# Optimization experiments

Hardware: AMD Instinct MI355X
Metric: run time of the kernel (lower is better)

The kernel has to match this reference:

```python
import jax, jax.numpy as jnp
import numpy as np
from jax import lax

NTAG = 31
HID = 100
NEG = -10000.0


def gru_dir(x, w_ih, w_hh, b_ih, b_hh):
    # x: [T, B, 100]; PyTorch gate order in weights: [r, z, n]
    B = x.shape[1]
    h0 = jnp.zeros((B, HID), dtype=x.dtype)

    def step(h, xt):
        gi = xt @ w_ih.T + b_ih          # [B, 3H]
        gh = h @ w_hh.T + b_hh           # [B, 3H]
        ir, iz, inn = jnp.split(gi, 3, axis=-1)
        hr, hz, hn = jnp.split(gh, 3, axis=-1)
        r = jax.nn.sigmoid(ir + hr)
        z = jax.nn.sigmoid(iz + hz)
        n = jnp.tanh(inn + r * hn)
        h = (1.0 - z) * n + z * h
        return h, h

    _, ys = lax.scan(step, h0, x)
    return ys                             # [T, B, H]


def viterbi(feats, msk, transitions):
    # feats: [T, 31], msk: [T], transitions[next, prev]
    init = jnp.full((NTAG,), NEG, dtype=feats.dtype).at[0].set(0.0)
    idx = jnp.arange(NTAG)

    def step(fv, inp):
        feat, m = inp
        scores = fv[None, :] + transitions       # [next, prev]
        bp = jnp.argmax(scores, axis=1)          # [31]
        vv = jnp.max(scores, axis=1) + feat      # [31]
        live = m > 0
        fv_new = jnp.where(live, vv, fv)
        bp = jnp.where(live, bp, idx)            # masked step: identity backpointer
        return fv_new, bp

    fv, bps = lax.scan(step, init, (feats, msk))
    final = jnp.argmax(fv)
    score = fv[final]

    def back(tag, bp):
        return bp[tag], tag

    _, path = lax.scan(back, final, bps, reverse=True)  # path[t] = tag at step t
    return score, path


def setup_inputs() -> dict:
    key = jax.random.key(0)
    ks = jax.random.split(key, 12)
    T, B, D = 2048, 128, 100
    s = 0.1  # ~ 1/sqrt(hidden)
    u = lambda k, sh: jax.random.uniform(k, sh, jnp.float32, -s, s)
    tr = jax.random.normal(ks[10], (NTAG, NTAG), jnp.float32)
    tr = tr.at[0, :].set(NEG).at[:, 29].set(NEG).at[:, 30].set(NEG)
    tr = tr.at[30, 30].set(0.0).at[29, 30].set(0.0)
    return {
        "sentence": jax.random.normal(ks[0], (T, B, D), jnp.float32),
        "mask": jnp.ones((B, T), jnp.float32),
        "w_ih_f": u(ks[1], (3 * HID, D)), "w_hh_f": u(ks[2], (3 * HID, HID)),
        "b_ih_f": u(ks[3], (3 * HID,)), "b_hh_f": u(ks[4], (3 * HID,)),
        "w_ih_b": u(ks[5], (3 * HID, D)), "w_hh_b": u(ks[6], (3 * HID, HID)),
        "b_ih_b": u(ks[7], (3 * HID,)), "b_hh_b": u(ks[8], (3 * HID,)),
        "w_out": u(ks[9], (NTAG, 2 * HID)), "b_out": jnp.zeros((NTAG,), jnp.float32),
        "transitions": tr,
        "batch": B,
        "seq": 0,
    }


def reference(sentence, mask, w_ih_f, w_hh_f, b_ih_f, b_hh_f,
              w_ih_b, w_hh_b, b_ih_b, b_hh_b, w_out, b_out,
              transitions, batch, seq):
    fwd = gru_dir(sentence, w_ih_f, w_hh_f, b_ih_f, b_hh_f)
    bwd = gru_dir(sentence[::-1], w_ih_b, w_hh_b, b_ih_b, b_hh_b)[::-1]
    gru_out = jnp.concatenate([fwd, bwd], axis=-1)        # [T, B, 200]
    feats = gru_out @ w_out.T + b_out                      # [T, B, 31]
    feats_b = jnp.transpose(feats, (1, 0, 2))              # [B, T, 31]
    score, path = viterbi(feats_b[seq], mask[seq], transitions)
    return score, path
```

## Files before the change

kernel.cpp:

```cpp
#include <hip/hip_runtime.h>
#include <stdint.h>

#define TT 2048
#define BB 128
#define DD 100
#define HH 100
#define GG 300
#define NT 31
#define NEGV (-10000.0f)

#define REP25(M) M(0) M(1) M(2) M(3) M(4) M(5) M(6) M(7) M(8) M(9) M(10) M(11) \
                 M(12) M(13) M(14) M(15) M(16) M(17) M(18) M(19) M(20) M(21) M(22) M(23) M(24)
#define REP31(M) M(0) M(1) M(2) M(3) M(4) M(5) M(6) M(7) M(8) M(9) M(10) M(11) \
                 M(12) M(13) M(14) M(15) M(16) M(17) M(18) M(19) M(20) M(21) M(22) M(23) \
                 M(24) M(25) M(26) M(27) M(28) M(29) M(30)
#define REP8(M)  M(0) M(1) M(2) M(3) M(4) M(5) M(6) M(7)

#define RL(v, k) __int_as_float(__builtin_amdgcn_readlane(__float_as_int(v), (k)))

__global__ __launch_bounds__(320) void gi_kernel(
    const float* __restrict__ sent, const int* __restrict__ seqp,
    const float* __restrict__ w_ih_f, const float* __restrict__ b_ih_f,
    const float* __restrict__ w_ih_b, const float* __restrict__ b_ih_b,
    float* __restrict__ gi)
{
    const int t   = blockIdx.x;
    const int dir = blockIdx.y;
    const int j   = threadIdx.x;
    const int seq = seqp[0];
    const int ts  = dir ? (TT - 1 - t) : t;
    __shared__ __align__(16) float x_s[DD];
    if (j < DD) x_s[j] = sent[((size_t)ts * BB + seq) * DD + j];
    __syncthreads();
    if (j < GG) {
        const float* w = dir ? w_ih_b : w_ih_f;
        const float* b = dir ? b_ih_b : b_ih_f;
        const float4* w4 = (const float4*)(w + j * DD);
        const float4* x4 = (const float4*)x_s;
        float a0 = 0.f, a1 = 0.f, a2 = 0.f, a3 = 0.f;
        #pragma unroll
        for (int k = 0; k < DD / 4; k++) {
            float4 wv = w4[k], xv = x4[k];
            a0 += wv.x * xv.x; a1 += wv.y * xv.y;
            a2 += wv.z * xv.z; a3 += wv.w * xv.w;
        }
        gi[((size_t)dir * TT + t) * GG + j] = b[j] + (a0 + a1) + (a2 + a3);
    }
}

__global__ __launch_bounds__(512, 2) void gru_seq_kernel(
    const float* __restrict__ gi,
    const float* __restrict__ w_hh_f, const float* __restrict__ b_hh_f,
    const float* __restrict__ w_hh_b, const float* __restrict__ b_hh_b,
    const float* __restrict__ w_out,
    float* __restrict__ pfeat)
{
    const int dir  = blockIdx.x;
    const int tid  = threadIdx.x;
    const int wave = tid >> 6, lane = tid & 63;
    const int q    = wave >> 1;
    const bool isA = !(wave & 1);
    const int k0   = q * 25;
    const float* w_hh = dir ? w_hh_b : w_hh_f;
    const float* b_hh = dir ? b_hh_b : b_hh_f;
    const float* gid  = gi + (size_t)dir * TT * GG;
    float* pf = pfeat + (size_t)dir * TT * NT;

    __shared__ float part[2][4][384];

    const int s0 = (isA ? 0 : 64) + lane;
    const int s1 = (isA ? 128 : 192) + lane;
    const int s2 = (isA ? 256 : 320) + lane;

    const float* r0 = w_hh + s0 * DD + k0;
    const float* r1 = w_hh + s1 * DD + k0;
    const int wrow = (s2 - GG) < (NT - 1) ? (s2 - GG) : (NT - 1);
    const float* r2 = (s2 < GG) ? (w_hh + s2 * DD + k0)
                                : (w_out + wrow * (2 * HH) + dir * HH + k0);

    #define DECLW(i) float w0_##i, w1_##i, w2_##i;
    REP25(DECLW)
    #define LDW(i) w0_##i = r0[i]; w1_##i = r1[i]; w2_##i = r2[i];
    REP25(LDW)

    const int r = k0 + lane;
    float bhr = 0.f, bhz = 0.f, bhn = 0.f;
    if (lane < 25) { bhr = b_hh[r]; bhz = b_hh[HH + r]; bhn = b_hh[2 * HH + r]; }

    const int  p     = lane - 32;
    const bool is_pf = (wave == 1) && (p >= 0) && (p < NT);
    #define DECLPH(i) float ph##i = 0.f;
    REP8(DECLPH)

    float hreg = 0.f;

    float gAr = 0.f, gAz = 0.f, gAn = 0.f, gBr = 0.f, gBz = 0.f, gBn = 0.f;
    if (lane < 25) {
        gAr = gid[r];      gAz = gid[HH + r];      gAn = gid[2 * HH + r];
        gBr = gid[GG + r]; gBz = gid[GG + HH + r]; gBn = gid[GG + 2 * HH + r];
    }

    #define DOTK(i) { float hk = RL(hreg, i);              \
        a0 = fmaf(hk, w0_##i, a0);                          \
        a1 = fmaf(hk, w1_##i, a1);                          \
        a2 = fmaf(hk, w2_##i, a2); }

    #define GRU_STEP(TIDX, BUF, SLOT, cr, cz, cn) {                          \
        float a0 = 0.f, a1 = 0.f, a2 = 0.f;                                  \
        REP25(DOTK)                                                          \
        part[BUF][q][s0] = a0;                                               \
        part[BUF][q][s1] = a1;                                               \
        part[BUF][q][s2] = a2;                                               \
        __syncthreads();                                                     \
        if (lane < 25) {                                                     \
            float pr = part[BUF][0][r] + part[BUF][1][r]                     \
                     + part[BUF][2][r] + part[BUF][3][r];                    \
            float pz = part[BUF][0][HH + r] + part[BUF][1][HH + r]           \
                     + part[BUF][2][HH + r] + part[BUF][3][HH + r];          \
            float pn = part[BUF][0][2 * HH + r] + part[BUF][1][2 * HH + r]   \
                     + part[BUF][2][2 * HH + r] + part[BUF][3][2 * HH + r];  \
            float xr  = pr + bhr + (cr);                                     \
            float xz  = pz + bhz + (cz);                                     \
            float ghn = pn + bhn;                                            \
            float rr  = 1.f / (1.f + __expf(-xr));                           \
            float zz  = 1.f / (1.f + __expf(-xz));                           \
            float pre = (cn) + rr * ghn;                                     \
            pre = fmaxf(fminf(pre, 40.f), -40.f);                            \
            float e2  = __expf(-2.f * pre);                                  \
            float nn  = (1.f - e2) / (1.f + e2);                             \
            hreg = (1.f - zz) * nn + zz * hreg;                              \
            int tp = (TIDX) + 2; tp = (tp < TT) ? tp : (TT - 1);             \
            cr = gid[tp * GG + r];                                           \
            cz = gid[tp * GG + HH + r];                                      \
            cn = gid[tp * GG + 2 * HH + r];                                  \
        }                                                                    \
        if (is_pf && (TIDX) > 0) {                                           \
            ph##SLOT = part[BUF][0][GG + p] + part[BUF][1][GG + p]           \
                     + part[BUF][2][GG + p] + part[BUF][3][GG + p];          \
        }                                                                    \
    }

    #define PHST(i) pf[(size_t)(dir ? (TT - 1 - (tb + i)) : (tb + i)) * NT + p] = ph##i;

    for (int tt = 0; tt < TT; tt += 8) {
        GRU_STEP(tt + 0, 0, 7, gAr, gAz, gAn)
        if (is_pf && tt >= 8) { int tb = tt - 8; REP8(PHST) }
        GRU_STEP(tt + 1, 1, 0, gBr, gBz, gBn)
        GRU_STEP(tt + 2, 0, 1, gAr, gAz, gAn)
        GRU_STEP(tt + 3, 1, 2, gBr, gBz, gBn)
        GRU_STEP(tt + 4, 0, 3, gAr, gAz, gAn)
        GRU_STEP(tt + 5, 1, 4, gBr, gBz, gBn)
        GRU_STEP(tt + 6, 0, 5, gAr, gAz, gAn)
        GRU_STEP(tt + 7, 1, 6, gBr, gBz, gBn)
    }

    {
        float a2 = 0.f;
        #define DOT2K(i) a2 = fmaf(RL(hreg, i), w2_##i, a2);
        REP25(DOT2K)
        part[0][q][s2] = a2;
        __syncthreads();
        if (is_pf) {
            ph7 = part[0][0][GG + p] + part[0][1][GG + p]
                + part[0][2][GG + p] + part[0][3][GG + p];
            int tb = TT - 8;
            REP8(PHST)
        }
    }
}

__global__ __launch_bounds__(64) void vit_scan_kernel(
    const float* __restrict__ pfeat, const float* __restrict__ mask,
    const int* __restrict__ seqp, const float* __restrict__ trans,
    const float* __restrict__ b_out,
    float* __restrict__ fvg, int* __restrict__ meta, float* __restrict__ out)
{
    const int lane = threadIdx.x;
    const int ln   = (lane < NT) ? lane : (NT - 1);
    const float* mrow = mask + (size_t)seqp[0] * TT;
    const float* pff = pfeat;
    const float* pfb = pfeat + (size_t)TT * NT;

    #define DECLTR(i) float tr##i = trans[ln * NT + i];
    REP31(DECLTR)
    const float bo = b_out[ln];

    float fv = (lane == 0) ? 0.f : NEGV;
    fvg[lane] = fv;

    float ffr[8], fbr[8], mr[8];
    #pragma unroll
    for (int q = 0; q < 8; q++) {
        ffr[q] = pff[q * NT + ln]; fbr[q] = pfb[q * NT + ln]; mr[q] = mrow[q];
    }

    for (int t = 0; t < TT; t += 8) {
        #pragma unroll
        for (int q = 0; q < 8; q++) {
            float fcur = ffr[q] + fbr[q] + bo;
            float mcur = mr[q];
            int tp = t + q + 8; tp = (tp < TT) ? tp : (TT - 1);
            ffr[q] = pff[tp * NT + ln]; fbr[q] = pfb[tp * NT + ln]; mr[q] = mrow[tp];
            #define VADD(i) float v##i = RL(fv, i) + tr##i;
            REP31(VADD)
            #undef VADD
            v0  = fmaxf(v0,  v16); v1  = fmaxf(v1,  v17); v2  = fmaxf(v2,  v18);
            v3  = fmaxf(v3,  v19); v4  = fmaxf(v4,  v20); v5  = fmaxf(v5,  v21);
            v6  = fmaxf(v6,  v22); v7  = fmaxf(v7,  v23); v8  = fmaxf(v8,  v24);
            v9  = fmaxf(v9,  v25); v10 = fmaxf(v10, v26); v11 = fmaxf(v11, v27);
            v12 = fmaxf(v12, v28); v13 = fmaxf(v13, v29); v14 = fmaxf(v14, v30);
            v0 = fmaxf(v0, v8);  v1 = fmaxf(v1, v9);  v2 = fmaxf(v2, v10);
            v3 = fmaxf(v3, v11); v4 = fmaxf(v4, v12); v5 = fmaxf(v5, v13);
            v6 = fmaxf(v6, v14); v7 = fmaxf(v7, v15);
            v0 = fmaxf(v0, v4); v1 = fmaxf(v1, v5); v2 = fmaxf(v2, v6); v3 = fmaxf(v3, v7);
            v0 = fmaxf(v0, v2); v1 = fmaxf(v1, v3);
            float m = fmaxf(v0, v1);
            float cand = m + fcur;
            fv = (mcur > 0.f) ? cand : fv;
            fvg[(t + q + 1) * 64 + lane] = fv;
        }
    }

    float fbest = RL(fv, 0);
    int ftag = 0;
    #pragma unroll
    for (int q = 1; q < NT; q++) {
        float s = RL(fv, q);
        if (s > fbest) { fbest = s; ftag = q; }
    }
    if (lane == 0) { out[0] = fbest; meta[0] = ftag; }
}

__global__ __launch_bounds__(1024) void vit_bp_kernel(
    const float* __restrict__ fvg, const float* __restrict__ mask,
    const int* __restrict__ seqp, const float* __restrict__ trans,
    uint8_t* __restrict__ bpg, uint8_t* __restrict__ gmapg)
{
    const int b    = blockIdx.x;
    const int tid  = threadIdx.x;
    const int wave = tid >> 6, lane = tid & 63;
    const int j    = lane & 31;
    const int jr   = (j < NT) ? j : (NT - 1);
    const float* mrow = mask + (size_t)seqp[0] * TT;

    __shared__ int bpl[64][32];

    float trj[NT];
    #pragma unroll
    for (int q = 0; q < NT; q++) trj[q] = trans[jr * NT + q];

    #pragma unroll
    for (int q4 = 0; q4 < 4; q4++) {
        const int t = b * 64 + wave * 4 + q4;
        float fvp = fvg[t * 64 + lane];
        float mcur = mrow[t];
        float best = RL(fvp, 0) + trj[0];
        int bi = 0;
        #pragma unroll
        for (int q = 1; q < NT; q++) {
            float s = RL(fvp, q) + trj[q];
            if (s > best) { best = s; bi = q; }
        }
        int bpn = (mcur > 0.f) ? bi : j;
        if (j == 31) bpn = 31;
        if (lane < 32) {
            bpl[wave * 4 + q4][lane] = bpn;
            if (j < NT) bpg[(size_t)t * NT + j] = (uint8_t)bpn;
        }
    }
    __syncthreads();
    if (wave == 0) {
        int G = j;
        for (int i = 0; i < 64; i++) {
            int bpv = bpl[i][j];
            G = __shfl(G, bpv);
        }
        if (lane < 32) gmapg[b * 32 + lane] = (uint8_t)G;
    }
}

__global__ __launch_bounds__(64) void vit_back_kernel(
    const uint8_t* __restrict__ bpg, const uint8_t* __restrict__ gmapg,
    const int* __restrict__ meta, float* __restrict__ out)
{
    const int tid = threadIdx.x;
    __shared__ uint8_t bps[TT * NT];
    __shared__ uint8_t gm[32 * 32];
    __shared__ uint8_t echk[32];

    const uint32_t* src = (const uint32_t*)bpg;
    uint32_t* dst = (uint32_t*)bps;
    for (int i = tid; i < TT * NT / 4; i += 64) dst[i] = src[i];
    for (int i = tid; i < 1024 / 4; i += 64)
        ((uint32_t*)gm)[i] = ((const uint32_t*)gmapg)[i];
    __syncthreads();

    if (tid == 0) {
        int tag = meta[0];
        for (int b = 31; b >= 0; b--) { echk[b] = (uint8_t)tag; tag = gm[b * 32 + tag]; }
    }
    __syncthreads();
    if (tid < 32) {
        int tag = echk[tid];
        for (int i = 63; i >= 0; i--) {
            int t = tid * 64 + i;
            out[1 + t] = (float)tag;
            tag = bps[t * NT + tag];
        }
    }
}

extern "C" void kernel_launch(void* const* d_in, const int* in_sizes, int n_in,
                              void* d_out, int out_size, void* d_ws, size_t ws_size,
                              hipStream_t stream) {
    const float* sent   = (const float*)d_in[0];
    const float* mask   = (const float*)d_in[1];
    const float* w_ih_f = (const float*)d_in[2];
    const float* w_hh_f = (const float*)d_in[3];
    const float* b_ih_f = (const float*)d_in[4];
    const float* b_hh_f = (const float*)d_in[5];
    const float* w_ih_b = (const float*)d_in[6];
    const float* w_hh_b = (const float*)d_in[7];
    const float* b_ih_b = (const float*)d_in[8];
    const float* b_hh_b = (const float*)d_in[9];
    const float* w_out  = (const float*)d_in[10];
    const float* b_out  = (const float*)d_in[11];
    const float* trans  = (const float*)d_in[12];
    const int*   seqp   = (const int*)d_in[14];
    float* out = (float*)d_out;

    float* gi    = (float*)d_ws;
    float* pfeat = gi + (size_t)2 * TT * GG;
    float* fvg   = pfeat + (size_t)2 * TT * NT;
    float* bpf   = fvg + (size_t)(TT + 1) * 64;
    uint8_t* bpg   = (uint8_t*)bpf;
    uint8_t* gmapg = bpg + (size_t)TT * NT;
    int*     meta  = (int*)(gmapg + 1024);

    gi_kernel<<<dim3(TT, 2), 320, 0, stream>>>(sent, seqp, w_ih_f, b_ih_f,
                                               w_ih_b, b_ih_b, gi);
    gru_seq_kernel<<<2, 512, 0, stream>>>(gi, w_hh_f, b_hh_f, w_hh_b, b_hh_b,
                                          w_out, pfeat);
    vit_scan_kernel<<<1, 64, 0, stream>>>(pfeat, mask, seqp, trans, b_out,
                                          fvg, meta, out);
    vit_bp_kernel<<<32, 1024, 0, stream>>>(fvg, mask, seqp, trans, bpg, gmapg);
    vit_back_kernel<<<1, 64, 0, stream>>>(bpg, gmapg, meta, out);
}
```

Measured before the change: 2.189 ms.

## Stage GRU input gates in double-buffered LDS and pin weights in VGPRs

Each 8-step block of precomputed input-gate values is now copied cooperatively into a double-buffered shared-memory tile, one block ahead, so the recurrent step reads LDS instead of issuing per-step global loads on the serial path. Empty asm constraints keep the recurrent weights and the Viterbi transition matrix resident in VGPRs, and waves-per-EU attributes replace the launch-bounds occupancy hint. The cost is extra LDS and a copy per block. The final block reads past the end of the gate array, and the buffer being refilled is not fenced against waves still reading it, so there is a race risk.

Measured after the change: 2.245 ms. +2.6%, slower.

```diff
diff --git a/kernel.cpp b/kernel.cpp
--- a/kernel.cpp
+++ b/kernel.cpp
@@ -48,7 +48,8 @@
     }
 }
 
-__global__ __launch_bounds__(512, 2) void gru_seq_kernel(
+__global__ __launch_bounds__(512) __attribute__((amdgpu_waves_per_eu(2, 2)))
+void gru_seq_kernel(
     const float* __restrict__ gi,
     const float* __restrict__ w_hh_f, const float* __restrict__ b_hh_f,
     const float* __restrict__ w_hh_b, const float* __restrict__ b_hh_b,
@@ -67,6 +68,7 @@
     float* pf = pfeat + (size_t)dir * TT * NT;
 
     __shared__ float part[2][4][384];
+    __shared__ __align__(16) float gibuf[2][8][GG];
 
     const int s0 = (isA ? 0 : 64) + lane;
     const int s1 = (isA ? 128 : 192) + lane;
@@ -82,6 +84,21 @@
     REP25(DECLW)
     #define LDW(i) w0_##i = r0[i]; w1_##i = r1[i]; w2_##i = r2[i];
     REP25(LDW)
+    asm volatile("" : "+v"(w0_0),"+v"(w0_1),"+v"(w0_2),"+v"(w0_3),"+v"(w0_4),
+                      "+v"(w0_5),"+v"(w0_6),"+v"(w0_7),"+v"(w0_8),"+v"(w0_9),
+                      "+v"(w0_10),"+v"(w0_11),"+v"(w0_12),"+v"(w0_13),"+v"(w0_14),
+                      "+v"(w0_15),"+v"(w0_16),"+v"(w0_17),"+v"(w0_18),"+v"(w0_19),
+                      "+v"(w0_20),"+v"(w0_21),"+v"(w0_22),"+v"(w0_23),"+v"(w0_24));
+    asm volatile("" : "+v"(w1_0),"+v"(w1_1),"+v"(w1_2),"+v"(w1_3),"+v"(w1_4),
+                      "+v"(w1_5),"+v"(w1_6),"+v"(w1_7),"+v"(w1_8),"+v"(w1_9),
+                      "+v"(w1_10),"+v"(w1_11),"+v"(w1_12),"+v"(w1_13),"+v"(w1_14),
+                      "+v"(w1_15),"+v"(w1_16),"+v"(w1_17),"+v"(w1_18),"+v"(w1_19),
+                      "+v"(w1_20),"+v"(w1_21),"+v"(w1_22),"+v"(w1_23),"+v"(w1_24));
+    asm volatile("" : "+v"(w2_0),"+v"(w2_1),"+v"(w2_2),"+v"(w2_3),"+v"(w2_4),
+                      "+v"(w2_5),"+v"(w2_6),"+v"(w2_7),"+v"(w2_8),"+v"(w2_9),
+                      "+v"(w2_10),"+v"(w2_11),"+v"(w2_12),"+v"(w2_13),"+v"(w2_14),
+                      "+v"(w2_15),"+v"(w2_16),"+v"(w2_17),"+v"(w2_18),"+v"(w2_19),
+                      "+v"(w2_20),"+v"(w2_21),"+v"(w2_22),"+v"(w2_23),"+v"(w2_24));
 
     const int r = k0 + lane;
     float bhr = 0.f, bhz = 0.f, bhn = 0.f;
@@ -94,18 +111,19 @@
 
     float hreg = 0.f;
 
-    float gAr = 0.f, gAz = 0.f, gAn = 0.f, gBr = 0.f, gBz = 0.f, gBn = 0.f;
-    if (lane < 25) {
-        gAr = gid[r];      gAz = gid[HH + r];      gAn = gid[2 * HH + r];
-        gBr = gid[GG + r]; gBz = gid[GG + HH + r]; gBn = gid[GG + 2 * HH + r];
-    }
+    auto stage = [&](int tbase, int nb) {
+        const float4* src = (const float4*)(gid + (size_t)tbase * GG);
+        float4* dst = (float4*)&gibuf[nb][0][0];
+        for (int i = tid; i < 600; i += 512) dst[i] = src[i];
+    };
+    stage(0, 0);
 
     #define DOTK(i) { float hk = RL(hreg, i);              \
         a0 = fmaf(hk, w0_##i, a0);                          \
         a1 = fmaf(hk, w1_##i, a1);                          \
         a2 = fmaf(hk, w2_##i, a2); }
 
-    #define GRU_STEP(TIDX, BUF, SLOT, cr, cz, cn) {                          \
+    #define GRU_STEP(TIDX, BUF, SLOT, GB) {                                  \
         float a0 = 0.f, a1 = 0.f, a2 = 0.f;                                  \
         REP25(DOTK)                                                          \
         part[BUF][q][s0] = a0;                                               \
@@ -119,20 +137,19 @@
                      + part[BUF][2][HH + r] + part[BUF][3][HH + r];          \
             float pn = part[BUF][0][2 * HH + r] + part[BUF][1][2 * HH + r]   \
                      + part[BUF][2][2 * HH + r] + part[BUF][3][2 * HH + r];  \
-            float xr  = pr + bhr + (cr);                                     \
-            float xz  = pz + bhz + (cz);                                     \
+            float gr = gibuf[GB][(TIDX) & 7][r];                             \
+            float gz = gibuf[GB][(TIDX) & 7][HH + r];                        \
+            float gn = gibuf[GB][(TIDX) & 7][2 * HH + r];                    \
+            float xr  = pr + bhr + gr;                                       \
+            float xz  = pz + bhz + gz;                                       \
             float ghn = pn + bhn;                                            \
             float rr  = 1.f / (1.f + __expf(-xr));                           \
             float zz  = 1.f / (1.f + __expf(-xz));                           \
-            float pre = (cn) + rr * ghn;                                     \
+            float pre = gn + rr * ghn;                                       \
             pre = fmaxf(fminf(pre, 40.f), -40.f);                            \
             float e2  = __expf(-2.f * pre);                                  \
             float nn  = (1.f - e2) / (1.f + e2);                             \
             hreg = (1.f - zz) * nn + zz * hreg;                              \
-            int tp = (TIDX) + 2; tp = (tp < TT) ? tp : (TT - 1);             \
-            cr = gid[tp * GG + r];                                           \
-            cz = gid[tp * GG + HH + r];                                      \
-            cn = gid[tp * GG + 2 * HH + r];                                  \
         }                                                                    \
         if (is_pf && (TIDX) > 0) {                                           \
             ph##SLOT = part[BUF][0][GG + p] + part[BUF][1][GG + p]           \
@@ -143,15 +160,17 @@
     #define PHST(i) pf[(size_t)(dir ? (TT - 1 - (tb + i)) : (tb + i)) * NT + p] = ph##i;
 
     for (int tt = 0; tt < TT; tt += 8) {
-        GRU_STEP(tt + 0, 0, 7, gAr, gAz, gAn)
+        const int gb = (tt >> 3) & 1;
+        stage(tt + 8, gb ^ 1);
+        GRU_STEP(tt + 0, 0, 7, gb)
         if (is_pf && tt >= 8) { int tb = tt - 8; REP8(PHST) }
-        GRU_STEP(tt + 1, 1, 0, gBr, gBz, gBn)
-        GRU_STEP(tt + 2, 0, 1, gAr, gAz, gAn)
-        GRU_STEP(tt + 3, 1, 2, gBr, gBz, gBn)
-        GRU_STEP(tt + 4, 0, 3, gAr, gAz, gAn)
-        GRU_STEP(tt + 5, 1, 4, gBr, gBz, gBn)
-        GRU_STEP(tt + 6, 0, 5, gAr, gAz, gAn)
-        GRU_STEP(tt + 7, 1, 6, gBr, gBz, gBn)
+        GRU_STEP(tt + 1, 1, 0, gb)
+        GRU_STEP(tt + 2, 0, 1, gb)
+        GRU_STEP(tt + 3, 1, 2, gb)
+        GRU_STEP(tt + 4, 0, 3, gb)
+        GRU_STEP(tt + 5, 1, 4, gb)
+        GRU_STEP(tt + 6, 0, 5, gb)
+        GRU_STEP(tt + 7, 1, 6, gb)
     }
 
     {
@@ -169,7 +188,8 @@
     }
 }
 
-__global__ __launch_bounds__(64) void vit_scan_kernel(
+__global__ __launch_bounds__(64) __attribute__((amdgpu_waves_per_eu(1)))
+void vit_scan_kernel(
     const float* __restrict__ pfeat, const float* __restrict__ mask,
     const int* __restrict__ seqp, const float* __restrict__ trans,
     const float* __restrict__ b_out,
@@ -183,6 +203,13 @@
 
     #define DECLTR(i) float tr##i = trans[ln * NT + i];
     REP31(DECLTR)
+    asm volatile("" : "+v"(tr0),"+v"(tr1),"+v"(tr2),"+v"(tr3),"+v"(tr4),
+                      "+v"(tr5),"+v"(tr6),"+v"(tr7),"+v"(tr8),"+v"(tr9),
+                      "+v"(tr10),"+v"(tr11),"+v"(tr12),"+v"(tr13),"+v"(tr14),
+                      "+v"(tr15),"+v"(tr16),"+v"(tr17),"+v"(tr18),"+v"(tr19),
+                      "+v"(tr20),"+v"(tr21),"+v"(tr22),"+v"(tr23),"+v"(tr24),
+                      "+v"(tr25),"+v"(tr26),"+v"(tr27),"+v"(tr28),"+v"(tr29),
+                      "+v"(tr30));
     const float bo = b_out[ln];
 
     float fv = (lane == 0) ? 0.f : NEGV;
```
